# Optimization experiments

Measured on AMD Instinct MI355X. Metric: run time of the kernel, lower is better.

## Reference

```python
import jax, jax.numpy as jnp
import numpy as np

H = 128  # target_size / hidden_size
D_IN = 2  # input_size - 2 (stard_LSTM slices off last 2 grid coords)
SAMP = 10  # sampling_num (hardcoded stride 10 in forward loop)


def lstm_encode(x, lengths, W_ih, W_hh, b_ih, b_hh):
    # x: [B, T, D_IN]; torch.nn.LSTMCell math, zero initial state
    B, T, _ = x.shape
    xg = jnp.einsum('btd,gd->btg', x, W_ih) + b_ih  # precompute input projections [B,T,4H]

    def step(carry, xt):
        h, c = carry
        g = xt + h @ W_hh.T + b_hh
        i, f, gg, o = jnp.split(g, 4, axis=-1)
        c = jax.nn.sigmoid(f) * c + jax.nn.sigmoid(i) * jnp.tanh(gg)
        h = jax.nn.sigmoid(o) * jnp.tanh(c)
        return (h, c), h

    h0 = jnp.zeros((B, H), x.dtype)
    _, hs = jax.lax.scan(step, (h0, h0), xg.transpose(1, 0, 2))
    outputs = hs.transpose(1, 0, 2)  # [B, T, H]
    emb = outputs[jnp.arange(B), jnp.clip(lengths - 1, 0)]  # last valid step per sequence
    return emb, outputs


def gather_sub(tensor, sub_len):
    # tensor: [B, T, H]; sub_len: [B*SAMP]; row k reads tensor[k//SAMP, sub_len[k]-1]
    rows = jnp.arange(sub_len.shape[0]) // SAMP
    return tensor[rows, jnp.clip(sub_len - 1, 0)]


def exp_neg_dist(a, b):
    return jnp.exp(-jnp.sqrt(jnp.sum((a - b) ** 2, axis=-1)))


def setup_inputs() -> dict:
    key = jax.random.key(0)
    ks = jax.random.split(key, 12)
    B, T, D = 220, 512, 4
    NS = B * SAMP
    rint = lambda k, n: jnp.maximum(jax.random.randint(k, (n,), 0, T), 1).astype(jnp.int64)
    inp = {
        'traj_input': jax.random.normal(ks[0], (B, T, D), jnp.float32),
        'traj_length': rint(ks[1], B),
        'traj_anchor_sub_length': rint(ks[2], NS),
        'traj_farest_sub_length': rint(ks[3], NS),
        'traj_anchor_input': jax.random.normal(ks[4], (B, T, D), jnp.float32),
        'traj_anchor_length': rint(ks[5], B),
        'anchor_sub_length': rint(ks[6], NS),
        'traj_farest_input': jax.random.normal(ks[7], (B, T, D), jnp.float32),
        'traj_farest_length': rint(ks[8], B),
        'farest_sub_length': rint(ks[9], NS),
        'W_ih': jax.random.normal(ks[10], (4 * H, D_IN), jnp.float32) / np.sqrt(H),
        'W_hh': jax.random.normal(ks[11], (4 * H, H), jnp.float32) / np.sqrt(H),
        'b_ih': jnp.zeros((4 * H,), jnp.float32),
        'b_hh': jnp.zeros((4 * H,), jnp.float32),
    }
    return inp


def reference(traj_input, traj_length, traj_anchor_sub_length, traj_farest_sub_length,
              traj_anchor_input, traj_anchor_length, anchor_sub_length,
              traj_farest_input, traj_farest_length, farest_sub_length,
              W_ih, W_hh, b_ih, b_hh):
    # stard_LSTM=True path: cell input drops last 2 coords
    t_emb, t_out = lstm_encode(traj_input[..., :-2], traj_length, W_ih, W_hh, b_ih, b_hh)
    a_emb, a_out = lstm_encode(traj_anchor_input[..., :-2], traj_anchor_length, W_ih, W_hh, b_ih, b_hh)
    f_emb, f_out = lstm_encode(traj_farest_input[..., :-2], traj_farest_length, W_ih, W_hh, b_ih, b_hh)

    ta_sub = gather_sub(t_out, traj_anchor_sub_length)
    tf_sub = gather_sub(t_out, traj_farest_sub_length)
    an_sub = gather_sub(a_out, anchor_sub_length)
    fa_sub = gather_sub(f_out, farest_sub_length)

    anchor_distance = exp_neg_dist(t_emb, a_emb)
    farest_distance = exp_neg_dist(t_emb, f_emb)
    anchor_sub_distance = exp_neg_dist(ta_sub, an_sub)
    farest_sub_distance = exp_neg_dist(tf_sub, fa_sub)
    return (anchor_distance, farest_distance, anchor_sub_distance, farest_sub_distance)
```

## Files before the change

### kernel.cpp

```cpp
#include <hip/hip_runtime.h>

#define H    128
#define T    512
#define DX   4
#define BB   220
#define SAMP 10
#define NS   (BB*SAMP)
#define M    4
#define NBLK 55
#define MAXSLOT 84

typedef _Float16 half8 __attribute__((ext_vector_type(8)));
typedef float    f32x4 __attribute__((ext_vector_type(4)));

#define WS_TEMB 0
#define WS_AEMB (WS_TEMB + BB*H)
#define WS_FEMB (WS_AEMB + BB*H)
#define WS_TA   (WS_FEMB + BB*H)
#define WS_TF   (WS_TA + NS*H)
#define WS_AN   (WS_TF + NS*H)
#define WS_FA   (WS_AN + NS*H)
#define WS_FLAGS (WS_FA + NS*H)

#define LOG2E  1.442695041f
#define LOG2E2 2.885390082f

__device__ static inline float bf2f(unsigned short u) {
  unsigned int i = ((unsigned int)u) << 16;
  return __builtin_bit_cast(float, i);
}
__device__ static inline unsigned short f2bf(float f) {
  unsigned int i = __builtin_bit_cast(unsigned int, f);
  i += 0x7fffu + ((i >> 16) & 1u);
  return (unsigned short)(i >> 16);
}
__device__ static inline float loadF(const void* p, size_t i, int isbf) {
  return isbf ? bf2f(((const unsigned short*)p)[i]) : ((const float*)p)[i];
}
__device__ static inline int loadI(const void* p, int i, int is64) {
  return is64 ? (int)((const unsigned int*)p)[2*(size_t)i] : ((const int*)p)[i];
}
__device__ static inline float frcp(float x) { return __builtin_amdgcn_rcpf(x); }
__device__ static inline float ex2(float x)  { return __builtin_amdgcn_exp2f(x); }
__device__ static inline float sigmY(float y)  { return frcp(1.f + ex2(-y)); }
__device__ static inline float tanhY(float y)  { return 1.f - 2.f*frcp(1.f + ex2(y)); }
__device__ static inline float scrub(float x) { return (x == x) ? x : 0.f; }
__device__ static inline int clampT(int v) { v = v - 1; if (v < 0) v = 0; if (v > T-1) v = T-1; return v; }

__global__ __launch_bounds__(256, 1) void lstm_scan(
    const void* __restrict__ x0_, const void* __restrict__ len0,
    const void* __restrict__ sub_ta, const void* __restrict__ sub_tf,
    const void* __restrict__ x1_, const void* __restrict__ len1,
    const void* __restrict__ sub_an,
    const void* __restrict__ x2_, const void* __restrict__ len2,
    const void* __restrict__ sub_fa,
    const void* __restrict__ Wih, const void* __restrict__ Whh,
    const void* __restrict__ bih, const void* __restrict__ bhh,
    float* __restrict__ ws)
{
  const int e      = blockIdx.y;
  const int s0     = blockIdx.x * M;
  const int tid    = threadIdx.x;
  const int lane   = tid & 63;
  const int w      = tid >> 6;
  const int lo     = lane & 15;
  const int quad   = lane >> 4;

  int fbf, f64;
  {
    const unsigned int* wp = (const unsigned int*)Whh;
    int cnt = 0;
    for (int i = 0; i < 64; ++i) {
      unsigned int lo16 = wp[i] & 0xFFFFu;
      int ex = (int)((lo16 >> 7) & 0xFFu);
      cnt += (ex >= 100 && ex <= 130);
    }
    fbf = (cnt >= 40);
    const unsigned int* l = (const unsigned int*)len0;
    f64 = ((l[1] | l[3] | l[5] | l[7]) == 0u);
    if (blockIdx.x == 0 && blockIdx.y == 0 && tid == 0) {
      int* fo = (int*)(ws + WS_FLAGS); fo[0] = fbf; fo[1] = f64;
    }
  }

  const void* xin  = (e==0) ? x0_ : (e==1 ? x1_ : x2_);
  const void* lenp = (e==0) ? len0 : (e==1 ? len1 : len2);

  __shared__ __align__(16) _Float16 afr[2][4][16][8];
  __shared__ __align__(16) float2 xbf[M][T+2];
  __shared__ __align__(16) _Float16 sbuf[MAXSLOT][H];
  __shared__ int slot_off[MAXSLOT];

  for (int i = tid; i < 512; i += 256) ((unsigned int*)afr)[i] = 0u;
  for (int i = tid; i < M*T; i += 256) {
    int m = i >> 9, t = i & (T-1);
    size_t base = ((size_t)(s0+m)*T + t) * DX;
    xbf[m][t] = make_float2(loadF(xin, base + 0, fbf), loadF(xin, base + 1, fbf));
  }
  half8 Bf[2][4][4];
  #pragma unroll
  for (int ch = 0; ch < 2; ++ch) {
    const int col = w*32 + ch*16 + lo;
    #pragma unroll
    for (int q = 0; q < 4; ++q) {
      const float sc = (q == 2) ? LOG2E2 : LOG2E;
      const int g = q*128 + col;
      #pragma unroll
      for (int kt = 0; kt < 4; ++kt) {
        #pragma unroll
        for (int j = 0; j < 8; ++j) {
          const int k = kt*32 + quad*8 + j;
          Bf[ch][q][kt][j] = (_Float16)(sc * loadF(Whh, (size_t)g*H + k, fbf));
        }
      }
    }
  }
  float wx0[2][4], wx1[2][4], bb[2][4];
  #pragma unroll
  for (int ch = 0; ch < 2; ++ch) {
    const int col = w*32 + ch*16 + lo;
    #pragma unroll
    for (int q = 0; q < 4; ++q) {
      const float sc = (q == 2) ? LOG2E2 : LOG2E;
      const int g = q*128 + col;
      wx0[ch][q] = sc * loadF(Wih, (size_t)g*2 + 0, fbf);
      wx1[ch][q] = sc * loadF(Wih, (size_t)g*2 + 1, fbf);
      bb[ch][q]  = sc * (loadF(bih, g, fbf) + loadF(bhh, g, fbf));
    }
  }
  const int nslots = (e == 0) ? M*21 : M*11;
  int myt = -2, mym = 0;
  if (e == 0) {
    if (tid < M*21) {
      int m = tid / 21, j = tid - m*21, sg = s0 + m;
      mym = m;
      int off;
      if (j == 0)       { myt = clampT(loadI(lenp, sg, f64));            off = WS_TEMB + sg*H; }
      else if (j <= 10) { int k = sg*10 + (j-1);  myt = clampT(loadI(sub_ta, k, f64)); off = WS_TA + k*H; }
      else              { int k = sg*10 + (j-11); myt = clampT(loadI(sub_tf, k, f64)); off = WS_TF + k*H; }
      slot_off[tid] = off;
    }
  } else {
    if (tid < M*11) {
      int m = tid / 11, j = tid - m*11, sg = s0 + m;
      mym = m;
      int off;
      if (j == 0) { myt = clampT(loadI(lenp, sg, f64)); off = (e==1 ? WS_AEMB : WS_FEMB) + sg*H; }
      else {
        int k = sg*10 + (j-1);
        if (e == 1) { myt = clampT(loadI(sub_an, k, f64)); off = WS_AN + k*H; }
        else        { myt = clampT(loadI(sub_fa, k, f64)); off = WS_FA + k*H; }
      }
      slot_off[tid] = off;
    }
  }
  __syncthreads();

  float cs[2] = {0.f, 0.f};
  const int rdchunk = quad*4 + (lo >> 2);
  const _Float16* rdb[2] = { &afr[0][0][rdchunk][0], &afr[1][0][rdchunk][0] };
  const _Float16* sbb[2] = { &afr[0][0][0][0], &afr[1][0][0][0] };
  _Float16* wrb[2][2] = {
    { &afr[0][w][((lo>>3)  )*4+quad][lo&7], &afr[0][w][(2+(lo>>3))*4+quad][lo&7] },
    { &afr[1][w][((lo>>3)  )*4+quad][lo&7], &afr[1][w][(2+(lo>>3))*4+quad][lo&7] } };
  const float2* xrow = &xbf[quad][0];
  const int c0 = 2*lane;
  const int snap_base = (c0 >> 5)*128 + ((c0 >> 3) & 3)*32 + (c0 & 7);

  auto snap = [&](int tq, int rp) {
    unsigned long long mask = __ballot(myt == tq);
    if (mask) {
      const _Float16* sb = sbb[rp];
      do {
        int src = __ffsll((unsigned long long)mask) - 1;
        mask &= mask - 1;
        int m    = __shfl(mym, src);
        int slot = w*64 + src;
        unsigned int pk = *(const unsigned int*)(sb + snap_base + m*8);
        *(unsigned int*)&sbuf[slot][c0] = pk;
      } while (mask);
    }
  };

  f32x4 G[2][4];
  float2 xn;
  {
    float2 v0 = xrow[0];
    #pragma unroll
    for (int ch = 0; ch < 2; ++ch)
      #pragma unroll
      for (int q = 0; q < 4; ++q)
        G[ch][q] = (f32x4){ bb[ch][q] + wx0[ch][q]*v0.x + wx1[ch][q]*v0.y, 0.f, 0.f, 0.f };
    xn = xrow[1];
  }

  auto step = [&](int rp, int wp, int t) {
    const _Float16* rb = rdb[rp];
    half8 A[4];
    #pragma unroll
    for (int kt = 0; kt < 4; ++kt)
      A[kt] = *(const half8*)(rb + kt*128);

    #pragma unroll
    for (int kt = 0; kt < 4; ++kt)
      #pragma unroll
      for (int ch = 0; ch < 2; ++ch)
        #pragma unroll
        for (int q = 0; q < 4; ++q)
          G[ch][q] = __builtin_amdgcn_mfma_f32_16x16x32_f16(A[kt], Bf[ch][q][kt], G[ch][q], 0, 0, 0);

    float pan[2][4];
    #pragma unroll
    for (int ch = 0; ch < 2; ++ch)
      #pragma unroll
      for (int q = 0; q < 4; ++q)
        pan[ch][q] = bb[ch][q] + wx0[ch][q]*xn.x + wx1[ch][q]*xn.y;
    xn = xrow[t+2];
    snap(t-1, rp);

    #pragma unroll
    for (int ch = 0; ch < 2; ++ch) {
      float sf = sigmY(G[ch][1][0]);
      float si = sigmY(G[ch][0][0]);
      float tg = tanhY(G[ch][2][0]);
      float ig = (si * tg) * LOG2E2;
      cs[ch] = sf*cs[ch] + ig;
      float tc = tanhY(cs[ch]);
      float so = sigmY(G[ch][3][0]);
      *wrb[wp][ch] = (_Float16)(so * tc);
    }
    #pragma unroll
    for (int ch = 0; ch < 2; ++ch)
      #pragma unroll
      for (int q = 0; q < 4; ++q)
        G[ch][q][0] = pan[ch][q];
    __syncthreads();
  };

  #pragma unroll 1
  for (int t = 0; t < T; t += 2) {
    step(0, 1, t);
    step(1, 0, t+1);
  }

  snap(T-1, 0);

  __syncthreads();
  for (int i = tid; i < nslots*64; i += 256) {
    int slot = i >> 6, c2 = i & 63;
    unsigned int pk = *(const unsigned int*)&sbuf[slot][2*c2];
    float2 v;
    v.x = (float)__builtin_bit_cast(_Float16, (unsigned short)(pk & 0xFFFFu));
    v.y = (float)__builtin_bit_cast(_Float16, (unsigned short)(pk >> 16));
    *(float2*)(ws + slot_off[slot] + 2*c2) = v;
  }
}

__global__ void dists(const float* __restrict__ ws, void* __restrict__ outv) {
  const int fbf = ((const int*)(ws + WS_FLAGS))[0];
  const int gtid = blockIdx.x*256 + threadIdx.x;
  const int widx = gtid >> 6, lane = gtid & 63;
  const float *pa, *pb;
  if (widx < 220)       { pa = ws + WS_TEMB + (size_t)widx*H;        pb = ws + WS_AEMB + (size_t)widx*H; }
  else if (widx < 440)  { int b = widx-220;  pa = ws + WS_TEMB + (size_t)b*H; pb = ws + WS_FEMB + (size_t)b*H; }
  else if (widx < 2640) { int k = widx-440;  pa = ws + WS_TA + (size_t)k*H;   pb = ws + WS_AN + (size_t)k*H; }
  else                  { int k = widx-2640; pa = ws + WS_TF + (size_t)k*H;   pb = ws + WS_FA + (size_t)k*H; }
  float d0 = pa[lane]    - pb[lane];
  float d1 = pa[lane+64] - pb[lane+64];
  float s  = scrub(d0*d0 + d1*d1);
  #pragma unroll
  for (int off = 32; off > 0; off >>= 1) s += __shfl_down(s, off, 64);
  if (lane == 0) {
    float r = __expf(-sqrtf(s));
    if (fbf) ((unsigned short*)outv)[widx] = f2bf(r);
    else     ((float*)outv)[widx] = r;
  }
}

extern "C" void kernel_launch(void* const* d_in, const int* in_sizes, int n_in,
                              void* d_out, int out_size, void* d_ws, size_t ws_size,
                              hipStream_t stream) {
  float* ws = (float*)d_ws;
  hipLaunchKernelGGL(lstm_scan, dim3(NBLK, 3), dim3(256), 0, stream,
                     d_in[0], d_in[1], d_in[2], d_in[3],
                     d_in[4], d_in[5], d_in[6],
                     d_in[7], d_in[8], d_in[9],
                     d_in[10], d_in[11], d_in[12], d_in[13], ws);
  hipLaunchKernelGGL(dists, dim3(4840*64/256), dim3(256), 0, stream, ws, d_out);
}
```

Measured before the change: 417.2 us.

## Swap MFMA operand roles to pack 16 sequences per block, stream inputs in chunks

The recurrent weights become the MFMA A operand, with gate rows interleaved, and the hidden state becomes the B operand. Each 16x16x32 MFMA now covers 16 sequences instead of leaving most rows idle, so each block processes 16 sequences with 512 threads. That halves the MFMAs per wave per timestep on the serial recurrence chain, and far fewer blocks are needed. Inputs are streamed through a double-buffered 64-step LDS chunk with register prefetch, and snapshots are written straight to global memory instead of being staged through an LDS slot buffer. The risks are extra barriers at chunk boundaries, a partially filled last block, and scattered global writes inside the time loop.

```diff
diff --git a/kernel.cpp b/kernel.cpp
--- a/kernel.cpp
+++ b/kernel.cpp
@@ -6,9 +6,9 @@
 #define BB   220
 #define SAMP 10
 #define NS   (BB*SAMP)
-#define M    4
-#define NBLK 55
-#define MAXSLOT 84
+#define M    16
+#define NBLK 14
+#define NCH  8
 
 typedef _Float16 half8 __attribute__((ext_vector_type(8)));
 typedef float    f32x4 __attribute__((ext_vector_type(4)));
@@ -47,7 +47,7 @@
 __device__ static inline float scrub(float x) { return (x == x) ? x : 0.f; }
 __device__ static inline int clampT(int v) { v = v - 1; if (v < 0) v = 0; if (v > T-1) v = T-1; return v; }
 
-__global__ __launch_bounds__(256, 1) void lstm_scan(
+__global__ __launch_bounds__(512, 1) void lstm_scan(
     const void* __restrict__ x0_, const void* __restrict__ len0,
     const void* __restrict__ sub_ta, const void* __restrict__ sub_tf,
     const void* __restrict__ x1_, const void* __restrict__ len1,
@@ -86,174 +86,219 @@
   const void* xin  = (e==0) ? x0_ : (e==1 ? x1_ : x2_);
   const void* lenp = (e==0) ? len0 : (e==1 ? len1 : len2);
 
-  __shared__ __align__(16) _Float16 afr[2][4][16][8];
-  __shared__ __align__(16) float2 xbf[M][T+2];
-  __shared__ __align__(16) _Float16 sbuf[MAXSLOT][H];
-  __shared__ int slot_off[MAXSLOT];
-
-  for (int i = tid; i < 512; i += 256) ((unsigned int*)afr)[i] = 0u;
-  for (int i = tid; i < M*T; i += 256) {
-    int m = i >> 9, t = i & (T-1);
-    size_t base = ((size_t)(s0+m)*T + t) * DX;
-    xbf[m][t] = make_float2(loadF(xin, base + 0, fbf), loadF(xin, base + 1, fbf));
-  }
-  half8 Bf[2][4][4];
-  #pragma unroll
-  for (int ch = 0; ch < 2; ++ch) {
-    const int col = w*32 + ch*16 + lo;
+  __shared__ __align__(16) _Float16 hb[2][4][4][16][8];
+  __shared__ __align__(16) float2 xc[2][16][65];
+
+  for (int i = tid; i < 2048; i += 512) ((unsigned int*)hb)[i] = 0u;
+
+  #pragma unroll
+  for (int k2 = 0; k2 < 2; ++k2) {
+    int i = tid + k2*512, seq = i >> 6, tl = i & 63, sg = s0 + seq;
+    float2 v = make_float2(0.f, 0.f);
+    if (sg < BB) {
+      size_t base = ((size_t)sg*T + tl) * DX;
+      v = make_float2(loadF(xin, base + 0, fbf), loadF(xin, base + 1, fbf));
+    }
+    xc[0][seq][tl] = v;
+  }
+  uint2 Rx[2];
+  #pragma unroll
+  for (int k2 = 0; k2 < 2; ++k2) {
+    int i = tid + k2*512, seq = i >> 6, tl = i & 63, sg = s0 + seq;
+    uint2 r = make_uint2(0u, 0u);
+    if (sg < BB) {
+      size_t base = ((size_t)sg*T + (64 + tl)) * DX;
+      if (fbf) r.x = *(const unsigned int*)((const unsigned short*)xin + base);
+      else { const unsigned int* pu = (const unsigned int*)xin; r.x = pu[base]; r.y = pu[base+1]; }
+    }
+    Rx[k2] = r;
+  }
+
+  half8 Af[4][4];
+  {
+    const int qw = lo & 3, hcl = lo >> 2;
+    const float sc = (qw == 2) ? LOG2E2 : LOG2E;
+    #pragma unroll
+    for (int rt = 0; rt < 4; ++rt) {
+      const size_t row = (size_t)(qw*128 + (w*4 + rt)*4 + hcl) * H;
+      #pragma unroll
+      for (int kt = 0; kt < 4; ++kt)
+        #pragma unroll
+        for (int j = 0; j < 8; ++j)
+          Af[rt][kt][j] = (_Float16)(sc * loadF(Whh, row + kt*32 + quad*8 + j, fbf));
+    }
+  }
+  float wx0[4][4], wx1[4][4], bbq[4][4];
+  #pragma unroll
+  for (int rt = 0; rt < 4; ++rt) {
+    const int hcc = (w*4 + rt)*4 + quad;
     #pragma unroll
     for (int q = 0; q < 4; ++q) {
       const float sc = (q == 2) ? LOG2E2 : LOG2E;
-      const int g = q*128 + col;
-      #pragma unroll
-      for (int kt = 0; kt < 4; ++kt) {
-        #pragma unroll
-        for (int j = 0; j < 8; ++j) {
-          const int k = kt*32 + quad*8 + j;
-          Bf[ch][q][kt][j] = (_Float16)(sc * loadF(Whh, (size_t)g*H + k, fbf));
-        }
-      }
-    }
-  }
-  float wx0[2][4], wx1[2][4], bb[2][4];
-  #pragma unroll
-  for (int ch = 0; ch < 2; ++ch) {
-    const int col = w*32 + ch*16 + lo;
-    #pragma unroll
-    for (int q = 0; q < 4; ++q) {
-      const float sc = (q == 2) ? LOG2E2 : LOG2E;
-      const int g = q*128 + col;
-      wx0[ch][q] = sc * loadF(Wih, (size_t)g*2 + 0, fbf);
-      wx1[ch][q] = sc * loadF(Wih, (size_t)g*2 + 1, fbf);
-      bb[ch][q]  = sc * (loadF(bih, g, fbf) + loadF(bhh, g, fbf));
-    }
-  }
-  const int nslots = (e == 0) ? M*21 : M*11;
-  int myt = -2, mym = 0;
+      const int g = q*128 + hcc;
+      wx0[rt][q] = sc * loadF(Wih, (size_t)g*2 + 0, fbf);
+      wx1[rt][q] = sc * loadF(Wih, (size_t)g*2 + 1, fbf);
+      bbq[rt][q] = sc * (loadF(bih, g, fbf) + loadF(bhh, g, fbf));
+    }
+  }
+  int myt = -2, mym = 0, myoff = 0;
   if (e == 0) {
     if (tid < M*21) {
       int m = tid / 21, j = tid - m*21, sg = s0 + m;
       mym = m;
-      int off;
-      if (j == 0)       { myt = clampT(loadI(lenp, sg, f64));            off = WS_TEMB + sg*H; }
-      else if (j <= 10) { int k = sg*10 + (j-1);  myt = clampT(loadI(sub_ta, k, f64)); off = WS_TA + k*H; }
-      else              { int k = sg*10 + (j-11); myt = clampT(loadI(sub_tf, k, f64)); off = WS_TF + k*H; }
-      slot_off[tid] = off;
+      if (sg < BB) {
+        if (j == 0)       { myt = clampT(loadI(lenp, sg, f64));            myoff = WS_TEMB + sg*H; }
+        else if (j <= 10) { int k = sg*10 + (j-1);  myt = clampT(loadI(sub_ta, k, f64)); myoff = WS_TA + k*H; }
+        else              { int k = sg*10 + (j-11); myt = clampT(loadI(sub_tf, k, f64)); myoff = WS_TF + k*H; }
+      }
     }
   } else {
     if (tid < M*11) {
       int m = tid / 11, j = tid - m*11, sg = s0 + m;
       mym = m;
-      int off;
-      if (j == 0) { myt = clampT(loadI(lenp, sg, f64)); off = (e==1 ? WS_AEMB : WS_FEMB) + sg*H; }
-      else {
-        int k = sg*10 + (j-1);
-        if (e == 1) { myt = clampT(loadI(sub_an, k, f64)); off = WS_AN + k*H; }
-        else        { myt = clampT(loadI(sub_fa, k, f64)); off = WS_FA + k*H; }
+      if (sg < BB) {
+        if (j == 0) { myt = clampT(loadI(lenp, sg, f64)); myoff = (e==1 ? WS_AEMB : WS_FEMB) + sg*H; }
+        else {
+          int k = sg*10 + (j-1);
+          if (e == 1) { myt = clampT(loadI(sub_an, k, f64)); myoff = WS_AN + k*H; }
+          else        { myt = clampT(loadI(sub_fa, k, f64)); myoff = WS_FA + k*H; }
+        }
       }
-      slot_off[tid] = off;
-    }
-  }
-  __syncthreads();
-
-  float cs[2] = {0.f, 0.f};
-  const int rdchunk = quad*4 + (lo >> 2);
-  const _Float16* rdb[2] = { &afr[0][0][rdchunk][0], &afr[1][0][rdchunk][0] };
-  const _Float16* sbb[2] = { &afr[0][0][0][0], &afr[1][0][0][0] };
-  _Float16* wrb[2][2] = {
-    { &afr[0][w][((lo>>3)  )*4+quad][lo&7], &afr[0][w][(2+(lo>>3))*4+quad][lo&7] },
-    { &afr[1][w][((lo>>3)  )*4+quad][lo&7], &afr[1][w][(2+(lo>>3))*4+quad][lo&7] } };
-  const float2* xrow = &xbf[quad][0];
+    }
+  }
+
+  const _Float16* hb0 = &hb[0][0][0][0][0];
+  const _Float16* hb1 = &hb[1][0][0][0][0];
+  const _Float16* rdb[2] = { hb0, hb1 };
+  const int rdoff = quad*128 + lo*8;
+  _Float16* wrp[2][4];
+  #pragma unroll
+  for (int rt = 0; rt < 4; ++rt) {
+    const int hcc = (w*4 + rt)*4 + quad;
+    const int offh = (hcc>>5)*512 + ((hcc>>3)&3)*128 + lo*8 + (hcc&7);
+    wrp[0][rt] = (_Float16*)hb0 + offh;
+    wrp[1][rt] = (_Float16*)hb1 + offh;
+  }
   const int c0 = 2*lane;
-  const int snap_base = (c0 >> 5)*128 + ((c0 >> 3) & 3)*32 + (c0 & 7);
+  const int snap_kb = (c0>>5)*512 + ((c0>>3)&3)*128 + (c0&7);
 
   auto snap = [&](int tq, int rp) {
     unsigned long long mask = __ballot(myt == tq);
     if (mask) {
-      const _Float16* sb = sbb[rp];
+      const _Float16* sb = rdb[rp];
       do {
         int src = __ffsll((unsigned long long)mask) - 1;
         mask &= mask - 1;
-        int m    = __shfl(mym, src);
-        int slot = w*64 + src;
-        unsigned int pk = *(const unsigned int*)(sb + snap_base + m*8);
-        *(unsigned int*)&sbuf[slot][c0] = pk;
+        int m   = __shfl(mym, src);
+        int off = __shfl(myoff, src);
+        unsigned int pk = *(const unsigned int*)(sb + snap_kb + m*8);
+        float2 v;
+        v.x = (float)__builtin_bit_cast(_Float16, (unsigned short)(pk & 0xFFFFu));
+        v.y = (float)__builtin_bit_cast(_Float16, (unsigned short)(pk >> 16));
+        *(float2*)(ws + off + c0) = v;
       } while (mask);
     }
   };
 
-  f32x4 G[2][4];
-  float2 xn;
+  __syncthreads();
+
+  f32x4 G[4];
+  float cs[4] = {0.f, 0.f, 0.f, 0.f};
   {
-    float2 v0 = xrow[0];
-    #pragma unroll
-    for (int ch = 0; ch < 2; ++ch)
+    float2 xv0 = xc[0][lo][0];
+    #pragma unroll
+    for (int rt = 0; rt < 4; ++rt)
       #pragma unroll
       for (int q = 0; q < 4; ++q)
-        G[ch][q] = (f32x4){ bb[ch][q] + wx0[ch][q]*v0.x + wx1[ch][q]*v0.y, 0.f, 0.f, 0.f };
-    xn = xrow[1];
-  }
-
-  auto step = [&](int rp, int wp, int t) {
-    const _Float16* rb = rdb[rp];
-    half8 A[4];
+        G[rt][q] = bbq[rt][q] + wx0[rt][q]*xv0.x + wx1[rt][q]*xv0.y;
+  }
+
+  auto step = [&](int rp, int wp, int t, bool last) {
+    const _Float16* rb = rdb[rp] + rdoff;
+    half8 Bh[4];
     #pragma unroll
     for (int kt = 0; kt < 4; ++kt)
-      A[kt] = *(const half8*)(rb + kt*128);
+      Bh[kt] = *(const half8*)(rb + kt*512);
+    float2 xn;
+    if (!last) xn = xc[(t>>6)&1][lo][(t+1)&63];
 
     #pragma unroll
     for (int kt = 0; kt < 4; ++kt)
       #pragma unroll
-      for (int ch = 0; ch < 2; ++ch)
+      for (int rt = 0; rt < 4; ++rt)
+        G[rt] = __builtin_amdgcn_mfma_f32_16x16x32_f16(Af[rt][kt], Bh[kt], G[rt], 0, 0, 0);
+
+    float pxn[4][4];
+    if (!last) {
+      #pragma unroll
+      for (int rt = 0; rt < 4; ++rt)
         #pragma unroll
         for (int q = 0; q < 4; ++q)
-          G[ch][q] = __builtin_amdgcn_mfma_f32_16x16x32_f16(A[kt], Bf[ch][q][kt], G[ch][q], 0, 0, 0);
-
-    float pan[2][4];
-    #pragma unroll
-    for (int ch = 0; ch < 2; ++ch)
-      #pragma unroll
-      for (int q = 0; q < 4; ++q)
-        pan[ch][q] = bb[ch][q] + wx0[ch][q]*xn.x + wx1[ch][q]*xn.y;
-    xn = xrow[t+2];
+          pxn[rt][q] = bbq[rt][q] + wx0[rt][q]*xn.x + wx1[rt][q]*xn.y;
+    }
     snap(t-1, rp);
 
     #pragma unroll
-    for (int ch = 0; ch < 2; ++ch) {
-      float sf = sigmY(G[ch][1][0]);
-      float si = sigmY(G[ch][0][0]);
-      float tg = tanhY(G[ch][2][0]);
+    for (int rt = 0; rt < 4; ++rt) {
+      float sf = sigmY(G[rt][1]);
+      float si = sigmY(G[rt][0]);
+      float tg = tanhY(G[rt][2]);
       float ig = (si * tg) * LOG2E2;
-      cs[ch] = sf*cs[ch] + ig;
-      float tc = tanhY(cs[ch]);
-      float so = sigmY(G[ch][3][0]);
-      *wrb[wp][ch] = (_Float16)(so * tc);
-    }
-    #pragma unroll
-    for (int ch = 0; ch < 2; ++ch)
-      #pragma unroll
-      for (int q = 0; q < 4; ++q)
-        G[ch][q][0] = pan[ch][q];
+      cs[rt] = sf*cs[rt] + ig;
+      float tc = tanhY(cs[rt]);
+      float so = sigmY(G[rt][3]);
+      *wrp[wp][rt] = (_Float16)(so * tc);
+    }
+    if (!last) {
+      #pragma unroll
+      for (int rt = 0; rt < 4; ++rt)
+        #pragma unroll
+        for (int q = 0; q < 4; ++q)
+          G[rt][q] = pxn[rt][q];
+    }
     __syncthreads();
   };
 
   #pragma unroll 1
   for (int t = 0; t < T; t += 2) {
-    step(0, 1, t);
-    step(1, 0, t+1);
+    step(0, 1, t, false);
+    step(1, 0, t+1, (t & 63) == 62);
+    if ((t & 63) == 62 && t + 2 < T) {
+      const int tb1 = (t >> 6) + 1;
+      #pragma unroll
+      for (int k2 = 0; k2 < 2; ++k2) {
+        int i = tid + k2*512, seq = i >> 6, tl = i & 63;
+        float2 v;
+        if (fbf) v = make_float2(bf2f((unsigned short)(Rx[k2].x & 0xFFFFu)),
+                                 bf2f((unsigned short)(Rx[k2].x >> 16)));
+        else     v = make_float2(__builtin_bit_cast(float, Rx[k2].x),
+                                 __builtin_bit_cast(float, Rx[k2].y));
+        xc[tb1 & 1][seq][tl] = v;
+      }
+      if (tb1 + 1 < NCH) {
+        #pragma unroll
+        for (int k2 = 0; k2 < 2; ++k2) {
+          int i = tid + k2*512, seq = i >> 6, tl = i & 63, sg = s0 + seq;
+          uint2 r = make_uint2(0u, 0u);
+          if (sg < BB) {
+            size_t base = ((size_t)sg*T + ((tb1 + 1)*64 + tl)) * DX;
+            if (fbf) r.x = *(const unsigned int*)((const unsigned short*)xin + base);
+            else { const unsigned int* pu = (const unsigned int*)xin; r.x = pu[base]; r.y = pu[base+1]; }
+          }
+          Rx[k2] = r;
+        }
+      }
+      __syncthreads();
+      float2 xv = xc[tb1 & 1][lo][0];
+      #pragma unroll
+      for (int rt = 0; rt < 4; ++rt)
+        #pragma unroll
+        for (int q = 0; q < 4; ++q)
+          G[rt][q] = bbq[rt][q] + wx0[rt][q]*xv.x + wx1[rt][q]*xv.y;
+    }
   }
 
   snap(T-1, 0);
-
-  __syncthreads();
-  for (int i = tid; i < nslots*64; i += 256) {
-    int slot = i >> 6, c2 = i & 63;
-    unsigned int pk = *(const unsigned int*)&sbuf[slot][2*c2];
-    float2 v;
-    v.x = (float)__builtin_bit_cast(_Float16, (unsigned short)(pk & 0xFFFFu));
-    v.y = (float)__builtin_bit_cast(_Float16, (unsigned short)(pk >> 16));
-    *(float2*)(ws + slot_off[slot] + 2*c2) = v;
-  }
 }
 
 __global__ void dists(const float* __restrict__ ws, void* __restrict__ outv) {
@@ -281,7 +326,7 @@
                               void* d_out, int out_size, void* d_ws, size_t ws_size,
                               hipStream_t stream) {
   float* ws = (float*)d_ws;
-  hipLaunchKernelGGL(lstm_scan, dim3(NBLK, 3), dim3(256), 0, stream,
+  hipLaunchKernelGGL(lstm_scan, dim3(NBLK, 3), dim3(512), 0, stream,
                      d_in[0], d_in[1], d_in[2], d_in[3],
                      d_in[4], d_in[5], d_in[6],
                      d_in[7], d_in[8], d_in[9],
```

After: 545.8 us. +30.8%, slower.
